# Performance work log

Measured on AMD Instinct MI355X. Metric: run time of the kernel, lower is better.

## Reference

```python
import jax, jax.numpy as jnp
import numpy as np

N = 50000   # nodes
F = 128     # num_features (per branch)
E = 800000  # edges
G = 16      # graphs in batch
T = 3       # blocks per branch


def setup_inputs() -> dict:
    key = jax.random.key(0)
    ks = jax.random.split(key, 32)
    s = 0.05
    d = {}
    d["x"] = jax.random.normal(ks[0], (N, 2 * F), jnp.float32)
    d["edge_index"] = jax.random.randint(ks[1], (2, E), 0, N)
    d["edge_weight"] = jax.random.uniform(ks[2], (E,), jnp.float32)
    d["batch"] = jnp.sort(jax.random.randint(ks[3], (N,), 0, G))
    d["states"] = jax.random.randint(ks[4], (N,), 0, 2).astype(jnp.float32)

    def w(k, shape):
        return jax.random.normal(k, shape, jnp.float32) * s

    for i, p in enumerate(["p1", "p2"]):
        b = 5 + i * 5
        d[f"{p}_a0"] = w(ks[b], (T,))            # alpha0: Linear(1,1,bias=False) weight per block
        d[f"{p}_a1W"] = w(ks[b + 1], (T, F, F))    # alpha1 weight
        d[f"{p}_a1b"] = w(ks[b + 2], (T, F))       # alpha1 bias
        d[f"{p}_linW"] = w(ks[b + 3], (T, F, F))   # conv.lin weight
        d[f"{p}_linb"] = w(ks[b + 4], (T, F))      # conv.lin bias
    d["beta0_W"] = w(ks[15], (F, F))
    d["beta1_W"] = w(ks[16], (F, F))
    d["beta2_W"] = w(ks[17], (F, 2 * F))
    d["beta2_b"] = w(ks[18], (F,))
    d["gamma0_W"] = w(ks[19], (F, F))
    d["gamma1_W"] = w(ks[20], (F, F))
    d["gamma2_W"] = w(ks[21], (F, F))
    d["gamma3_W"] = w(ks[22], (3 * F // 2, 3 * F))
    d["gamma4_W"] = w(ks[23], (1, 3 * F // 2))
    d["gamma4_b"] = w(ks[24], (1,))
    return d


def _lrelu(v):
    return jax.nn.leaky_relu(v, 0.2)


def _block(x, states, a0, a1W, a1b, linW, linb, src, dst, ew):
    # x = lrelu(alpha1(x + alpha0(states)))
    h = _lrelu((x + states[:, None] * a0) @ a1W.T + a1b)
    # CustomGCNConv: lin then edge-weighted gather/scatter-add (source->target)
    h = h @ linW.T + linb
    msg = ew[:, None] * h[src]  # [E, F]
    return jax.ops.segment_sum(msg, dst, num_segments=x.shape[0])


def reference(x, edge_index, edge_weight, batch, states,
              p1_a0, p1_a1W, p1_a1b, p1_linW, p1_linb,
              p2_a0, p2_a1W, p2_a1b, p2_linW, p2_linb,
              beta0_W, beta1_W, beta2_W, beta2_b,
              gamma0_W, gamma1_W, gamma2_W, gamma3_W, gamma4_W, gamma4_b):
    Fh = x.shape[1] // 2
    x1, x2 = x[:, :Fh], x[:, Fh:]
    s0, s1 = edge_index[0], edge_index[1]
    x1s = jnp.zeros_like(x1)
    x2s = jnp.zeros_like(x2)
    for t in range(T):
        # branch1 uses reversed edges edge_index[[1,0]]
        x1 = _lrelu(_block(x1, states, p1_a0[t], p1_a1W[t], p1_a1b[t],
                           p1_linW[t], p1_linb[t], s1, s0, edge_weight))
        x2 = _lrelu(_block(x2, states, p2_a0[t], p2_a1W[t], p2_a1b[t],
                           p2_linW[t], p2_linb[t], s0, s1, edge_weight))
        x1s = x1s + x1
        x2s = x2s + x2
    xc = _lrelu(jnp.concatenate([x1s @ beta0_W.T, x2s @ beta1_W.T], -1) @ beta2_W.T + beta2_b)
    sel = (states == 1.0)[:, None]
    # per-graph pooled sums broadcast back to nodes (== repeat_interleave since batch is sorted)
    x_s = jax.ops.segment_sum(jnp.where(sel, xc, 0.0), batch, num_segments=G)[batch]
    x_sum = jax.ops.segment_sum(xc, batch, num_segments=G)[batch]
    h = jnp.concatenate([xc @ gamma0_W.T, x_s @ gamma1_W.T, x_sum @ gamma2_W.T], -1)
    h = _lrelu(h @ gamma3_W.T)
    return (h @ gamma4_W.T + gamma4_b).reshape(-1)
```

## Files before the change

kernel.cpp:

```cpp
#include <hip/hip_runtime.h>

typedef short s8v __attribute__((ext_vector_type(8)));
typedef float f32x4 __attribute__((ext_vector_type(4)));

#define LRELU(v) ((v) > 0.f ? (v) : 0.2f * (v))

constexpr int NBK = 391;
constexpr int TILE = 8192;
constexpr int CAP = 4096;

__device__ __forceinline__ float b2f(unsigned short b) {
  return __uint_as_float(((unsigned int)b) << 16);
}
__device__ __forceinline__ unsigned short f2b(float f) {
  unsigned int x = __float_as_uint(f);
  x += 0x7fffu + ((x >> 16) & 1u);
  return (unsigned short)(x >> 16);
}
__device__ __forceinline__ unsigned int pack2(float lo, float hi) {
  return ((unsigned int)f2b(hi) << 16) | (unsigned int)f2b(lo);
}

struct BArgs {
  const unsigned short* A1[2];
  const unsigned short* A2[2];
  int ldA1, ldA2, K1;
  const unsigned short* W[2];
  const float* bias[2];
  const float* a0p[2];
  const float* rowsum[2];
  unsigned short* C[2];
  const float* states;
  int N, K;
};

template<int FOUT, int ACT, bool HAS_BIAS, bool HAS_STATES>
__global__ __launch_bounds__(256) void bgemm(BArgs ba)
{
  constexpr int NF = FOUT / 16;
  __shared__ __align__(16) unsigned short Ws[FOUT * 128];
  const int d = blockIdx.y;
  const unsigned short* __restrict__ A1 = ba.A1[d];
  const unsigned short* __restrict__ A2 = ba.A2[d];
  const unsigned short* __restrict__ W  = ba.W[d];
  unsigned short* __restrict__ C = ba.C[d];
  const int N = ba.N, K = ba.K, K1 = ba.K1, ldA1 = ba.ldA1, ldA2 = ba.ldA2;

  const int tid = threadIdx.x;
  const int lane = tid & 63;
  const int w = tid >> 6;
  const int l15 = lane & 15;
  const int g = lane >> 4;
  const int m0 = blockIdx.x * 128;

  f32x4 zero4 = {0.f, 0.f, 0.f, 0.f};
  f32x4 acc[2][NF];
#pragma unroll
  for (int mf = 0; mf < 2; ++mf)
#pragma unroll
    for (int nf = 0; nf < NF; ++nf) acc[mf][nf] = zero4;

  for (int kk = 0; kk < K; kk += 128) {
#pragma unroll
    for (int j = 0; j < NF; ++j) {
      int idx = tid + j * 256;
      int o = idx >> 4, c = idx & 15;
      uint4 v = *(const uint4*)(W + (size_t)o * K + kk + c * 8);
      *(uint4*)&Ws[o * 128 + (c ^ (o & 15)) * 8] = v;
    }
    const unsigned short* Ap; int ldA, koff;
    if (kk < K1) { Ap = A1; ldA = ldA1; koff = kk; }
    else         { Ap = A2; ldA = ldA2; koff = kk - K1; }
    s8v a[2][4];
#pragma unroll
    for (int mf = 0; mf < 2; ++mf) {
      int row = m0 + w * 32 + mf * 16 + l15;
      const unsigned short* ar = Ap + (size_t)row * ldA + koff + g * 8;
#pragma unroll
      for (int ks = 0; ks < 4; ++ks) {
        s8v t = {};
        if (row < N) t = *(const s8v*)(ar + ks * 32);
        a[mf][ks] = t;
      }
    }
    __syncthreads();
#pragma unroll
    for (int ks = 0; ks < 4; ++ks) {
#pragma unroll
      for (int nf = 0; nf < NF; ++nf) {
        int c = ks * 4 + g;
        s8v b = *(const s8v*)&Ws[(nf * 16 + l15) * 128 + (c ^ l15) * 8];
        acc[0][nf] = __builtin_amdgcn_mfma_f32_16x16x32_bf16(a[0][ks], b, acc[0][nf], 0, 0, 0);
        acc[1][nf] = __builtin_amdgcn_mfma_f32_16x16x32_bf16(a[1][ks], b, acc[1][nf], 0, 0, 0);
      }
    }
    if (kk + 128 < K) __syncthreads();
  }

  const float a0 = HAS_STATES ? ba.a0p[d][0] : 0.f;
#pragma unroll
  for (int mf = 0; mf < 2; ++mf) {
#pragma unroll
    for (int r = 0; r < 4; ++r) {
      int row = m0 + w * 32 + mf * 16 + g * 4 + r;
      if (row >= N) continue;
      float sa = HAS_STATES ? ba.states[row] * a0 : 0.f;
      unsigned short* crow = C + (size_t)row * FOUT;
#pragma unroll
      for (int nf = 0; nf < NF; ++nf) {
        int col = nf * 16 + l15;
        float v = acc[mf][nf][r];
        if (HAS_BIAS) v += ba.bias[d][col];
        if (HAS_STATES) v += sa * ba.rowsum[d][col];
        if (ACT) v = LRELU(v);
        crow[col] = f2b(v);
      }
    }
  }
}

struct FArgs {
  const unsigned short* X[2];
  const unsigned short* W1[2];
  const float* b1[2];
  const float* a0p[2];
  const float* rowsum[2];
  const unsigned short* W2[2];
  const float* b2[2];
  unsigned short* H[2];
  const float* states;
  int N;
};

__global__ __launch_bounds__(256) void fused_mlp_kernel(FArgs fa)
{
  __shared__ __align__(16) unsigned short Ws[128 * 128];
  __shared__ __align__(16) unsigned short Tp[128 * 128];
  const int d = blockIdx.y;
  const int tid = threadIdx.x;
  const int lane = tid & 63;
  const int w = tid >> 6;
  const int l15 = lane & 15;
  const int g = lane >> 4;
  const int m0 = blockIdx.x * 128;
  const int N = fa.N;

#pragma unroll
  for (int j = 0; j < 8; ++j) {
    int idx = tid + j * 256;
    int o = idx >> 4, c = idx & 15;
    uint4 v = *(const uint4*)(fa.W1[d] + (size_t)o * 128 + c * 8);
    *(uint4*)&Ws[o * 128 + (c ^ (o & 15)) * 8] = v;
  }
  s8v a[2][4];
#pragma unroll
  for (int mf = 0; mf < 2; ++mf) {
    int row = m0 + w * 32 + mf * 16 + l15;
    const unsigned short* ar = fa.X[d] + (size_t)row * 128 + g * 8;
#pragma unroll
    for (int ks = 0; ks < 4; ++ks) {
      s8v t = {};
      if (row < N) t = *(const s8v*)(ar + ks * 32);
      a[mf][ks] = t;
    }
  }
  f32x4 zero4 = {0.f, 0.f, 0.f, 0.f};
  f32x4 acc[2][8];
#pragma unroll
  for (int mf = 0; mf < 2; ++mf)
#pragma unroll
    for (int nf = 0; nf < 8; ++nf) acc[mf][nf] = zero4;
  __syncthreads();
#pragma unroll
  for (int ks = 0; ks < 4; ++ks) {
#pragma unroll
    for (int nf = 0; nf < 8; ++nf) {
      int c = ks * 4 + g;
      s8v b = *(const s8v*)&Ws[(nf * 16 + l15) * 128 + (c ^ l15) * 8];
      acc[0][nf] = __builtin_amdgcn_mfma_f32_16x16x32_bf16(a[0][ks], b, acc[0][nf], 0, 0, 0);
      acc[1][nf] = __builtin_amdgcn_mfma_f32_16x16x32_bf16(a[1][ks], b, acc[1][nf], 0, 0, 0);
    }
  }
  const float a0 = fa.a0p[d][0];
#pragma unroll
  for (int mf = 0; mf < 2; ++mf) {
#pragma unroll
    for (int r = 0; r < 4; ++r) {
      int lrow = w * 32 + mf * 16 + g * 4 + r;
      int row = m0 + lrow;
      float sa = (row < N) ? fa.states[row] * a0 : 0.f;
#pragma unroll
      for (int nf = 0; nf < 8; ++nf) {
        int col = nf * 16 + l15;
        float v = 0.f;
        if (row < N) {
          v = acc[mf][nf][r] + fa.b1[d][col] + sa * fa.rowsum[d][col];
          v = LRELU(v);
        }
        int cch = col >> 3;
        Tp[lrow * 128 + ((cch ^ (lrow & 15)) << 3) + (col & 7)] = f2b(v);
      }
    }
  }
  __syncthreads();
#pragma unroll
  for (int j = 0; j < 8; ++j) {
    int idx = tid + j * 256;
    int o = idx >> 4, c = idx & 15;
    uint4 v = *(const uint4*)(fa.W2[d] + (size_t)o * 128 + c * 8);
    *(uint4*)&Ws[o * 128 + (c ^ (o & 15)) * 8] = v;
  }
  __syncthreads();
#pragma unroll
  for (int mf = 0; mf < 2; ++mf) {
    int lrow = w * 32 + mf * 16 + l15;
#pragma unroll
    for (int ks = 0; ks < 4; ++ks) {
      int c2 = ks * 4 + g;
      a[mf][ks] = *(const s8v*)&Tp[lrow * 128 + ((c2 ^ (lrow & 15)) << 3)];
    }
  }
#pragma unroll
  for (int mf = 0; mf < 2; ++mf)
#pragma unroll
    for (int nf = 0; nf < 8; ++nf) acc[mf][nf] = zero4;
#pragma unroll
  for (int ks = 0; ks < 4; ++ks) {
#pragma unroll
    for (int nf = 0; nf < 8; ++nf) {
      int c = ks * 4 + g;
      s8v b = *(const s8v*)&Ws[(nf * 16 + l15) * 128 + (c ^ l15) * 8];
      acc[0][nf] = __builtin_amdgcn_mfma_f32_16x16x32_bf16(a[0][ks], b, acc[0][nf], 0, 0, 0);
      acc[1][nf] = __builtin_amdgcn_mfma_f32_16x16x32_bf16(a[1][ks], b, acc[1][nf], 0, 0, 0);
    }
  }
#pragma unroll
  for (int mf = 0; mf < 2; ++mf) {
#pragma unroll
    for (int r = 0; r < 4; ++r) {
      int row = m0 + w * 32 + mf * 16 + g * 4 + r;
      if (row >= N) continue;
      unsigned short* crow = fa.H[d] + (size_t)row * 128;
#pragma unroll
      for (int nf = 0; nf < 8; ++nf) {
        int col = nf * 16 + l15;
        crow[col] = f2b(acc[mf][nf][r] + fa.b2[d][col]);
      }
    }
  }
}

__global__ __launch_bounds__(256) void g3_kernel(
    const unsigned short* __restrict__ wbuf,
    const unsigned short* __restrict__ A16,
    const unsigned short* __restrict__ B16,
    const int* __restrict__ batch,
    const unsigned short* __restrict__ W,
    const float* __restrict__ g4W,
    const float* __restrict__ g4b,
    float* __restrict__ out, int N)
{
  constexpr int NF = 12;
  __shared__ __align__(16) unsigned short Ws[192 * 128];
  const int tid = threadIdx.x;
  const int lane = tid & 63;
  const int w = tid >> 6;
  const int l15 = lane & 15;
  const int g = lane >> 4;
  const int m0 = blockIdx.x * 128;

  f32x4 zero4 = {0.f, 0.f, 0.f, 0.f};
  f32x4 acc[2][NF];
#pragma unroll
  for (int mf = 0; mf < 2; ++mf)
#pragma unroll
    for (int nf = 0; nf < NF; ++nf) acc[mf][nf] = zero4;

  int brow[2];
#pragma unroll
  for (int mf = 0; mf < 2; ++mf) {
    int row = m0 + w * 32 + mf * 16 + l15;
    brow[mf] = (row < N) ? batch[row] : 0;
  }

  for (int kk = 0; kk < 384; kk += 128) {
#pragma unroll
    for (int j = 0; j < NF; ++j) {
      int idx = tid + j * 256;
      int o = idx >> 4, c = idx & 15;
      uint4 v = *(const uint4*)(W + (size_t)o * 384 + kk + c * 8);
      *(uint4*)&Ws[o * 128 + (c ^ (o & 15)) * 8] = v;
    }
    s8v a[2][4];
#pragma unroll
    for (int mf = 0; mf < 2; ++mf) {
      int row = m0 + w * 32 + mf * 16 + l15;
      const unsigned short* ar;
      if (kk == 0)        ar = wbuf + (size_t)row * 128 + g * 8;
      else if (kk == 128) ar = A16 + (size_t)brow[mf] * 128 + g * 8;
      else                ar = B16 + (size_t)brow[mf] * 128 + g * 8;
#pragma unroll
      for (int ks = 0; ks < 4; ++ks) {
        s8v t = {};
        if (row < N) t = *(const s8v*)(ar + ks * 32);
        a[mf][ks] = t;
      }
    }
    __syncthreads();
#pragma unroll
    for (int ks = 0; ks < 4; ++ks) {
#pragma unroll
      for (int nf = 0; nf < NF; ++nf) {
        int c = ks * 4 + g;
        s8v b = *(const s8v*)&Ws[(nf * 16 + l15) * 128 + (c ^ l15) * 8];
        acc[0][nf] = __builtin_amdgcn_mfma_f32_16x16x32_bf16(a[0][ks], b, acc[0][nf], 0, 0, 0);
        acc[1][nf] = __builtin_amdgcn_mfma_f32_16x16x32_bf16(a[1][ks], b, acc[1][nf], 0, 0, 0);
      }
    }
    if (kk < 256) __syncthreads();
  }

  float w4[NF];
#pragma unroll
  for (int nf = 0; nf < NF; ++nf) w4[nf] = g4W[nf * 16 + l15];
  const float gb = g4b[0];

#pragma unroll
  for (int mf = 0; mf < 2; ++mf) {
#pragma unroll
    for (int r = 0; r < 4; ++r) {
      int row = m0 + w * 32 + mf * 16 + g * 4 + r;
      float dot = 0.f;
#pragma unroll
      for (int nf = 0; nf < NF; ++nf) {
        float v = acc[mf][nf][r];
        v = LRELU(v);
        dot += v * w4[nf];
      }
#pragma unroll
      for (int m = 1; m < 16; m <<= 1) dot += __shfl_xor(dot, m, 16);
      if (l15 == 0 && row < N) out[row] = dot + gb;
    }
  }
}

struct CJobs { const float* s[9]; unsigned short* d[9]; int n[9]; };
__global__ void convert_kernel(CJobs jb) {
  int j = blockIdx.y;
  int idx = (blockIdx.x * 256 + threadIdx.x) * 8;
  if (idx >= jb.n[j]) return;
  const float* s = jb.s[j] + idx;
  float4 p0 = *(const float4*)s;
  float4 p1 = *(const float4*)(s + 4);
  uint4 u;
  u.x = pack2(p0.x, p0.y); u.y = pack2(p0.z, p0.w);
  u.z = pack2(p1.x, p1.y); u.w = pack2(p1.z, p1.w);
  *(uint4*)(jb.d[j] + idx) = u;
}

__global__ void rowsum_kernel(const float* __restrict__ a1,
                              const float* __restrict__ a2, float* __restrict__ rs) {
  int j = blockIdx.x;
  const float* src = (j < 3) ? (a1 + (size_t)j * 16384) : (a2 + (size_t)(j - 3) * 16384);
  int o = threadIdx.x;
  float s = 0.f;
  for (int k = 0; k < 128; ++k) s += src[o * 128 + k];
  rs[j * 128 + o] = s;
}

__global__ void init_kernel(const float* __restrict__ x,
                            unsigned short* __restrict__ x1, unsigned short* __restrict__ x2,
                            int n)
{
  int idx = blockIdx.x * blockDim.x + threadIdx.x;
  int total = n * 16;
  for (; idx < total; idx += gridDim.x * blockDim.x) {
    int r = idx >> 4, c = idx & 15;
    const float* xr = x + (size_t)r * 256 + c * 8;
    float4 p0 = *(const float4*)xr;
    float4 p1 = *(const float4*)(xr + 4);
    uint4 u1;
    u1.x = pack2(p0.x, p0.y); u1.y = pack2(p0.z, p0.w);
    u1.z = pack2(p1.x, p1.y); u1.w = pack2(p1.z, p1.w);
    float4 q0 = *(const float4*)(xr + 128);
    float4 q1 = *(const float4*)(xr + 132);
    uint4 u2;
    u2.x = pack2(q0.x, q0.y); u2.y = pack2(q0.z, q0.w);
    u2.z = pack2(q1.x, q1.y); u2.w = pack2(q1.z, q1.w);
    ((uint4*)(x1 + (size_t)r * 128))[c] = u1;
    ((uint4*)(x2 + (size_t)r * 128))[c] = u2;
  }
}

struct S3Args { const unsigned int* a[2]; const unsigned int* b[2]; const unsigned int* c[2];
                unsigned int* o[2]; int n; };
__global__ void sum3_kernel(S3Args s)
{
  int d = blockIdx.y;
  const unsigned int* __restrict__ pa = s.a[d];
  const unsigned int* __restrict__ pb = s.b[d];
  const unsigned int* __restrict__ pc = s.c[d];
  unsigned int* __restrict__ po = s.o[d];
  for (int i = blockIdx.x * 256 + threadIdx.x; i < s.n; i += gridDim.x * 256) {
    unsigned int ua = pa[i], ub = pb[i], uc = pc[i];
    float lo = b2f((unsigned short)ua) + b2f((unsigned short)ub) + b2f((unsigned short)uc);
    float hi = b2f((unsigned short)(ua >> 16)) + b2f((unsigned short)(ub >> 16))
             + b2f((unsigned short)(uc >> 16));
    po[i] = pack2(lo, hi);
  }
}

struct BinArgs {
  const int* s0; const int* s1; const float* ew;
  int* bcur0; int* bcur1;
  unsigned long long* bin0; unsigned long long* bin1;
  int E;
};
__global__ __launch_bounds__(256) void bin_kernel(BinArgs ba)
{
  __shared__ int hist0[NBK], hist1[NBK];
  __shared__ int base0[NBK], base1[NBK];
  const int t = threadIdx.x;
  const int e0 = blockIdx.x * TILE;
  const int e1 = min(e0 + TILE, ba.E);
  for (int i = t; i < NBK; i += 256) { hist0[i] = 0; hist1[i] = 0; }
  __syncthreads();
  for (int e = e0 + t; e < e1; e += 256) {
    atomicAdd(&hist0[ba.s0[e] >> 7], 1);
    atomicAdd(&hist1[ba.s1[e] >> 7], 1);
  }
  __syncthreads();
  for (int i = t; i < NBK; i += 256) {
    int c0 = hist0[i];
    base0[i] = c0 ? atomicAdd(&ba.bcur0[i], c0) : 0;
    int c1 = hist1[i];
    base1[i] = c1 ? atomicAdd(&ba.bcur1[i], c1) : 0;
  }
  __syncthreads();
  for (int i = t; i < NBK; i += 256) { hist0[i] = 0; hist1[i] = 0; }
  __syncthreads();
  for (int e = e0 + t; e < e1; e += 256) {
    int d0 = ba.s0[e], d1 = ba.s1[e];
    unsigned long long wb = (unsigned long long)__float_as_uint(ba.ew[e]) << 32;
    int b0 = d0 >> 7, b1 = d1 >> 7;
    int r0 = base0[b0] + atomicAdd(&hist0[b0], 1);
    if (r0 < CAP)
      ba.bin0[(size_t)b0 * CAP + r0] = wb | (unsigned int)((d0 & 127) << 16) | (unsigned int)d1;
    int r1 = base1[b1] + atomicAdd(&hist1[b1], 1);
    if (r1 < CAP)
      ba.bin1[(size_t)b1 * CAP + r1] = wb | (unsigned int)((d1 & 127) << 16) | (unsigned int)d0;
  }
}

struct BScanArgs { const int* cnt[2]; int* bbase[2]; };
__global__ __launch_bounds__(128) void bscan_kernel(BScanArgs a)
{
  __shared__ int ld[2][NBK];
  int wid = threadIdx.x >> 6, lane = threadIdx.x & 63;
  for (int i = lane; i < NBK; i += 64) ld[wid][i] = a.cnt[wid][i];
  __syncthreads();
  if (lane == 0) {
    int acc = 0;
    for (int i = 0; i < NBK; ++i) { int v = ld[wid][i]; ld[wid][i] = acc; acc += v; }
    a.bbase[wid][NBK] = acc;
  }
  __syncthreads();
  for (int i = lane; i < NBK; i += 64) a.bbase[wid][i] = ld[wid][i];
}

struct RArgs {
  const int* bbase[2];
  const unsigned long long* bin[2];
  unsigned int* comb[2];
  int* row[2];
  int n;
};
__global__ __launch_bounds__(256) void reorder_kernel(RArgs ra)
{
  const int d = blockIdx.y;
  const int b = blockIdx.x;
  const unsigned long long* __restrict__ bin = ra.bin[d] + (size_t)b * CAP;
  unsigned int* __restrict__ comb = ra.comb[d];
  int* __restrict__ row = ra.row[d];
  const int nb = b * 128;
  const int ne = min(nb + 128, ra.n);
  const int t = threadIdx.x;
  __shared__ int lcnt[128];
  __shared__ int lcur[128];
  __shared__ int wtot[4];
  if (t < 128) lcnt[t] = 0;
  const int span_beg = ra.bbase[d][b];
  const int span_end = ra.bbase[d][b + 1];
  const int cnt = span_end - span_beg;
  __syncthreads();
  for (int i = t; i < cnt; i += 256) {
    int nl = ((unsigned int)bin[i] >> 16) & 127;
    atomicAdd(&lcnt[nl], 1);
  }
  __syncthreads();
  int lane = t & 63, wv = t >> 6;
  int v = (t < 128) ? lcnt[t] : 0;
  int sc = v;
#pragma unroll
  for (int off = 1; off < 64; off <<= 1) {
    int u = __shfl_up(sc, off, 64);
    if (lane >= off) sc += u;
  }
  if (lane == 63) wtot[wv] = sc;
  __syncthreads();
  int excl = sc - v + ((wv == 1) ? wtot[0] : 0);
  if (t < 128) {
    lcur[t] = excl;
    if (nb + t < ne) row[nb + t] = span_beg + excl;
  }
  if (b == NBK - 1 && t == 0) row[ra.n] = span_end;
  __syncthreads();
  for (int i = t; i < cnt; i += 256) {
    unsigned long long r = bin[i];
    unsigned int lo = (unsigned int)r;
    float w = __uint_as_float((unsigned int)(r >> 32));
    int nl = (lo >> 16) & 127;
    int slot = atomicAdd(&lcur[nl], 1);
    comb[span_beg + slot] = (lo & 0xffffu) | ((unsigned int)f2b(w) << 16);
  }
}

struct GArgs {
  const int* rowstart[2];
  const unsigned int* comb[2];
  const unsigned short* h[2];
  unsigned short* xout[2];
  int n;
};
__global__ void gather_kernel(GArgs ga)
{
  int gw = blockIdx.x * (blockDim.x >> 6) + (threadIdx.x >> 6);
  int lane = threadIdx.x & 63;
  if (gw >= 2 * ga.n) return;
  int dir = (gw >= ga.n) ? 1 : 0;
  int node = gw - dir * ga.n;
  const int* __restrict__ rowstart = ga.rowstart[dir];
  const unsigned int* __restrict__ comb = ga.comb[dir];
  const unsigned int* __restrict__ h = (const unsigned int*)ga.h[dir];
  int beg = rowstart[node], end = rowstart[node + 1];
  float a0 = 0.f, a1 = 0.f;
  for (int p = beg; p < end; p += 16) {
    unsigned int cc[16];
    unsigned int uu[16];
#pragma unroll
    for (int i = 0; i < 16; ++i) {
      int pi = p + i;
      cc[i] = (pi < end) ? comb[pi] : 0u;
    }
#pragma unroll
    for (int i = 0; i < 16; ++i)
      uu[i] = h[(size_t)(cc[i] & 0xffffu) * 64 + lane];
#pragma unroll
    for (int i = 0; i < 16; ++i) {
      float wv = b2f((unsigned short)(cc[i] >> 16));
      a0 += wv * b2f((unsigned short)uu[i]);
      a1 += wv * b2f((unsigned short)(uu[i] >> 16));
    }
  }
  float v0 = LRELU(a0), v1 = LRELU(a1);
  unsigned int* xo = (unsigned int*)(ga.xout[dir] + (size_t)node * 128);
  xo[lane] = pack2(v0, v1);
}

__global__ __launch_bounds__(256) void segsum_kernel(
    const unsigned short* __restrict__ xc, const int* __restrict__ batch,
    const float* __restrict__ states,
    float* __restrict__ gsel, float* __restrict__ gsum, int n)
{
  int slot = threadIdx.x >> 6;
  int lane = threadIdx.x & 63;
  int r0 = blockIdx.x * 128 + slot * 32;
  if (r0 >= n) return;
  int r1 = min(r0 + 32, n);
  const unsigned int* __restrict__ xcu = (const unsigned int*)xc;
  float sel0 = 0.f, sel1 = 0.f, sum0 = 0.f, sum1 = 0.f;
  int cur = batch[r0];
  for (int r = r0; r < r1; r += 4) {
    unsigned int u[4]; int bb[4]; float st[4];
#pragma unroll
    for (int i = 0; i < 4; ++i) {
      int ri = min(r + i, r1 - 1);
      u[i] = xcu[(size_t)ri * 64 + lane];
      bb[i] = batch[ri];
      st[i] = states[ri];
    }
    int m = min(4, r1 - r);
#pragma unroll
    for (int i = 0; i < 4; ++i) {
      if (i >= m) break;
      if (bb[i] != cur) {
        atomicAdd(&gsel[cur * 128 + lane * 2], sel0);
        atomicAdd(&gsel[cur * 128 + lane * 2 + 1], sel1);
        atomicAdd(&gsum[cur * 128 + lane * 2], sum0);
        atomicAdd(&gsum[cur * 128 + lane * 2 + 1], sum1);
        sel0 = sel1 = sum0 = sum1 = 0.f;
        cur = bb[i];
      }
      float lo = b2f((unsigned short)u[i]);
      float hi = b2f((unsigned short)(u[i] >> 16));
      sum0 += lo; sum1 += hi;
      if (st[i] == 1.0f) { sel0 += lo; sel1 += hi; }
    }
  }
  atomicAdd(&gsel[cur * 128 + lane * 2], sel0);
  atomicAdd(&gsel[cur * 128 + lane * 2 + 1], sel1);
  atomicAdd(&gsum[cur * 128 + lane * 2], sum0);
  atomicAdd(&gsum[cur * 128 + lane * 2 + 1], sum1);
}

__global__ void small16_kernel(const float* __restrict__ gsel, const float* __restrict__ gsum,
                               const float* __restrict__ g1W, const float* __restrict__ g2W,
                               unsigned short* __restrict__ A16, unsigned short* __restrict__ B16)
{
  int r = blockIdx.x, t = threadIdx.x, o = t & 127;
  const float* src = (t < 128) ? gsel : gsum;
  const float* Wm  = (t < 128) ? g1W : g2W;
  float acc = 0.f;
  for (int k = 0; k < 128; ++k) acc += src[r * 128 + k] * Wm[o * 128 + k];
  unsigned short* dst = (t < 128) ? A16 : B16;
  dst[r * 128 + o] = f2b(acc);
}

extern "C" void kernel_launch(void* const* d_in, const int* in_sizes, int n_in,
                              void* d_out, int out_size, void* d_ws, size_t ws_size,
                              hipStream_t stream)
{
  const int N = 50000, F = 128, E = 800000, G = 16, T = 3;
  const float* x      = (const float*)d_in[0];
  const int*   ei     = (const int*)d_in[1];
  const int*   s0     = ei;
  const int*   s1     = ei + E;
  const float* ew     = (const float*)d_in[2];
  const int*   batch  = (const int*)d_in[3];
  const float* states = (const float*)d_in[4];
  const float* p_a0[2]   = {(const float*)d_in[5],  (const float*)d_in[10]};
  const float* p_a1W[2]  = {(const float*)d_in[6],  (const float*)d_in[11]};
  const float* p_a1b[2]  = {(const float*)d_in[7],  (const float*)d_in[12]};
  const float* p_linW[2] = {(const float*)d_in[8],  (const float*)d_in[13]};
  const float* p_linb[2] = {(const float*)d_in[9],  (const float*)d_in[14]};
  const float* beta0W = (const float*)d_in[15];
  const float* beta1W = (const float*)d_in[16];
  const float* beta2W = (const float*)d_in[17];
  const float* beta2b = (const float*)d_in[18];
  const float* g0W = (const float*)d_in[19];
  const float* g1W = (const float*)d_in[20];
  const float* g2W = (const float*)d_in[21];
  const float* g3W = (const float*)d_in[22];
  const float* g4W = (const float*)d_in[23];
  const float* g4b = (const float*)d_in[24];
  float* out = (float*)d_out;

  char* p = (char*)d_ws;
  auto alloc = [&](size_t bytes) {
    char* r = p;
    p += (bytes + 255) & ~(size_t)255;
    return r;
  };
  const size_t NFb2 = (size_t)N * F * sizeof(unsigned short);
  unsigned short* X1[3] = {(unsigned short*)alloc(NFb2), (unsigned short*)alloc(NFb2),
                           (unsigned short*)alloc(NFb2)};
  unsigned short* X2[3] = {(unsigned short*)alloc(NFb2), (unsigned short*)alloc(NFb2),
                           (unsigned short*)alloc(NFb2)};
  unsigned short* TMP0 = (unsigned short*)alloc(NFb2);
  unsigned short* TMP1 = (unsigned short*)alloc(NFb2);
  unsigned short* HH0  = (unsigned short*)alloc(NFb2);
  unsigned short* HH1  = (unsigned short*)alloc(NFb2);
  int*   row0 = (int*)alloc((size_t)(N + 1) * 4);
  int*   row1 = (int*)alloc((size_t)(N + 1) * 4);
  int*   bbase0 = (int*)alloc((size_t)(NBK + 1) * 4);
  int*   bbase1 = (int*)alloc((size_t)(NBK + 1) * 4);
  int*   bcur0 = (int*)alloc((size_t)NBK * 4);
  int*   bcur1 = (int*)alloc((size_t)NBK * 4);
  unsigned long long* bin0 = (unsigned long long*)alloc((size_t)NBK * CAP * 8);
  unsigned long long* bin1 = (unsigned long long*)alloc((size_t)NBK * CAP * 8);
  unsigned int* comb0 = (unsigned int*)alloc((size_t)E * 4);
  unsigned int* comb1 = (unsigned int*)alloc((size_t)E * 4);
  float* gsel = (float*)alloc((size_t)G * F * 4);
  float* gsum = (float*)alloc((size_t)G * F * 4);
  unsigned short* A16b = (unsigned short*)alloc((size_t)G * F * 2);
  unsigned short* B16b = (unsigned short*)alloc((size_t)G * F * 2);
  unsigned short* wreg = (unsigned short*)alloc((size_t)352256 * 2);
  float* rs = (float*)alloc((size_t)6 * 128 * 4);

  unsigned short* a1Wb[2]  = {wreg + 0,      wreg + 49152};
  unsigned short* linWb[2] = {wreg + 98304,  wreg + 147456};
  unsigned short* b0b = wreg + 196608;
  unsigned short* b1b = wreg + 212992;
  unsigned short* b2b = wreg + 229376;
  unsigned short* g0b = wreg + 262144;
  unsigned short* g3b = wreg + 278528;

  const dim3 blk256(256);
  const int GX = (N + 127) / 128;
  const int KBIG = 1 << 30;
  const int EB = (E + TILE - 1) / TILE;

  hipMemsetAsync(bcur0, 0, (size_t)NBK * 4, stream);
  hipMemsetAsync(bcur1, 0, (size_t)NBK * 4, stream);
  BinArgs bna;
  bna.s0 = s0; bna.s1 = s1; bna.ew = ew;
  bna.bcur0 = bcur0; bna.bcur1 = bcur1;
  bna.bin0 = bin0; bna.bin1 = bin1;
  bna.E = E;
  bin_kernel<<<EB, blk256, 0, stream>>>(bna);
  BScanArgs bsa;
  bsa.cnt[0] = bcur0; bsa.cnt[1] = bcur1;
  bsa.bbase[0] = bbase0; bsa.bbase[1] = bbase1;
  bscan_kernel<<<1, 128, 0, stream>>>(bsa);
  RArgs ra;
  ra.bbase[0] = bbase0; ra.bbase[1] = bbase1;
  ra.bin[0] = bin0; ra.bin[1] = bin1;
  ra.comb[0] = comb0; ra.comb[1] = comb1;
  ra.row[0] = row0; ra.row[1] = row1;
  ra.n = N;
  reorder_kernel<<<dim3(NBK, 2), blk256, 0, stream>>>(ra);

  CJobs jb;
  jb.s[0] = p_a1W[0];  jb.d[0] = a1Wb[0];  jb.n[0] = 49152;
  jb.s[1] = p_a1W[1];  jb.d[1] = a1Wb[1];  jb.n[1] = 49152;
  jb.s[2] = p_linW[0]; jb.d[2] = linWb[0]; jb.n[2] = 49152;
  jb.s[3] = p_linW[1]; jb.d[3] = linWb[1]; jb.n[3] = 49152;
  jb.s[4] = beta0W;    jb.d[4] = b0b;      jb.n[4] = 16384;
  jb.s[5] = beta1W;    jb.d[5] = b1b;      jb.n[5] = 16384;
  jb.s[6] = beta2W;    jb.d[6] = b2b;      jb.n[6] = 32768;
  jb.s[7] = g0W;       jb.d[7] = g0b;      jb.n[7] = 16384;
  jb.s[8] = g3W;       jb.d[8] = g3b;      jb.n[8] = 73728;
  convert_kernel<<<dim3(36, 9), blk256, 0, stream>>>(jb);
  rowsum_kernel<<<6, 128, 0, stream>>>(p_a1W[0], p_a1W[1], rs);
  init_kernel<<<3125, blk256, 0, stream>>>(x, X1[0], X2[0], N);

  for (int t = 0; t < T; ++t) {
    int rv = t % 3, wv = (t + 1) % 3;

    FArgs fa;
    fa.X[0] = X1[rv];  fa.X[1] = X2[rv];
    fa.W1[0] = a1Wb[0] + t * 16384;  fa.W1[1] = a1Wb[1] + t * 16384;
    fa.b1[0] = p_a1b[0] + t * F;     fa.b1[1] = p_a1b[1] + t * F;
    fa.a0p[0] = p_a0[0] + t;         fa.a0p[1] = p_a0[1] + t;
    fa.rowsum[0] = rs + t * 128;     fa.rowsum[1] = rs + (3 + t) * 128;
    fa.W2[0] = linWb[0] + t * 16384; fa.W2[1] = linWb[1] + t * 16384;
    fa.b2[0] = p_linb[0] + t * F;    fa.b2[1] = p_linb[1] + t * F;
    fa.H[0] = HH0;  fa.H[1] = HH1;
    fa.states = states;  fa.N = N;
    fused_mlp_kernel<<<dim3(GX, 2), blk256, 0, stream>>>(fa);

    GArgs ga;
    ga.rowstart[0] = row0; ga.rowstart[1] = row1;
    ga.comb[0] = comb0;    ga.comb[1] = comb1;
    ga.h[0] = HH0;         ga.h[1] = HH1;
    ga.xout[0] = X1[wv];   ga.xout[1] = X2[wv];
    ga.n = N;
    gather_kernel<<<(2 * N + 3) / 4, blk256, 0, stream>>>(ga);
  }

  S3Args s3;
  s3.a[0] = (const unsigned int*)X1[0]; s3.b[0] = (const unsigned int*)X1[1];
  s3.c[0] = (const unsigned int*)X1[2]; s3.o[0] = (unsigned int*)TMP0;
  s3.a[1] = (const unsigned int*)X2[0]; s3.b[1] = (const unsigned int*)X2[1];
  s3.c[1] = (const unsigned int*)X2[2]; s3.o[1] = (unsigned int*)TMP1;
  s3.n = N * 64;
  sum3_kernel<<<dim3(2048, 2), blk256, 0, stream>>>(s3);

  BArgs bu;
  bu.A1[0] = TMP0; bu.A2[0] = TMP0; bu.A1[1] = TMP1; bu.A2[1] = TMP1;
  bu.ldA1 = 128; bu.ldA2 = 128; bu.K1 = KBIG;
  bu.W[0] = b0b; bu.W[1] = b1b;
  bu.bias[0] = nullptr; bu.bias[1] = nullptr;
  bu.a0p[0] = nullptr; bu.a0p[1] = nullptr;
  bu.rowsum[0] = nullptr; bu.rowsum[1] = nullptr;
  bu.C[0] = HH0; bu.C[1] = HH1;
  bu.states = nullptr; bu.N = N; bu.K = 128;
  bgemm<128, 0, false, false><<<dim3(GX, 2), blk256, 0, stream>>>(bu);

  BArgs b2a;
  b2a.A1[0] = HH0; b2a.A2[0] = HH1; b2a.A1[1] = nullptr; b2a.A2[1] = nullptr;
  b2a.ldA1 = 128; b2a.ldA2 = 128; b2a.K1 = 128;
  b2a.W[0] = b2b; b2a.W[1] = nullptr;
  b2a.bias[0] = beta2b; b2a.bias[1] = nullptr;
  b2a.a0p[0] = nullptr; b2a.a0p[1] = nullptr;
  b2a.rowsum[0] = nullptr; b2a.rowsum[1] = nullptr;
  b2a.C[0] = TMP0; b2a.C[1] = nullptr;
  b2a.states = nullptr; b2a.N = N; b2a.K = 256;
  bgemm<128, 1, true, false><<<dim3(GX, 1), blk256, 0, stream>>>(b2a);

  hipMemsetAsync(gsel, 0, (size_t)G * F * 4, stream);
  hipMemsetAsync(gsum, 0, (size_t)G * F * 4, stream);
  segsum_kernel<<<GX, blk256, 0, stream>>>(TMP0, batch, states, gsel, gsum, N);
  small16_kernel<<<G, blk256, 0, stream>>>(gsel, gsum, g1W, g2W, A16b, B16b);

  BArgs g0a;
  g0a.A1[0] = TMP0; g0a.A2[0] = TMP0; g0a.A1[1] = nullptr; g0a.A2[1] = nullptr;
  g0a.ldA1 = 128; g0a.ldA2 = 128; g0a.K1 = KBIG;
  g0a.W[0] = g0b; g0a.W[1] = nullptr;
  g0a.bias[0] = nullptr; g0a.bias[1] = nullptr;
  g0a.a0p[0] = nullptr; g0a.a0p[1] = nullptr;
  g0a.rowsum[0] = nullptr; g0a.rowsum[1] = nullptr;
  g0a.C[0] = TMP1; g0a.C[1] = nullptr;
  g0a.states = nullptr; g0a.N = N; g0a.K = 128;
  bgemm<128, 0, false, false><<<dim3(GX, 1), blk256, 0, stream>>>(g0a);

  g3_kernel<<<GX, blk256, 0, stream>>>(TMP1, A16b, B16b, batch, g3b, g4W, g4b, out, N);
}
```

Measured before the change: 468.2 us.

## Fuse tail GEMMs and fold block-sum into last gather

Three tail changes. The three-way branch sum moves into the final gather kernel, which adds the two earlier block outputs before writing. The two per-branch beta GEMMs and the beta2 GEMM become one kernel that keeps intermediates in shared memory. The gamma0 GEMM is fused into g3_kernel through an LDS tile. This removes several kernel launches and multiple N×128 bf16 round trips to global memory, at the cost of larger shared-memory use per block (about 96 KB in the beta kernel) and possibly lower occupancy.

```diff
diff --git a/kernel.cpp b/kernel.cpp
--- a/kernel.cpp
+++ b/kernel.cpp
@@ -19,104 +19,6 @@
 }
 __device__ __forceinline__ unsigned int pack2(float lo, float hi) {
   return ((unsigned int)f2b(hi) << 16) | (unsigned int)f2b(lo);
-}
-
-struct BArgs {
-  const unsigned short* A1[2];
-  const unsigned short* A2[2];
-  int ldA1, ldA2, K1;
-  const unsigned short* W[2];
-  const float* bias[2];
-  const float* a0p[2];
-  const float* rowsum[2];
-  unsigned short* C[2];
-  const float* states;
-  int N, K;
-};
-
-template<int FOUT, int ACT, bool HAS_BIAS, bool HAS_STATES>
-__global__ __launch_bounds__(256) void bgemm(BArgs ba)
-{
-  constexpr int NF = FOUT / 16;
-  __shared__ __align__(16) unsigned short Ws[FOUT * 128];
-  const int d = blockIdx.y;
-  const unsigned short* __restrict__ A1 = ba.A1[d];
-  const unsigned short* __restrict__ A2 = ba.A2[d];
-  const unsigned short* __restrict__ W  = ba.W[d];
-  unsigned short* __restrict__ C = ba.C[d];
-  const int N = ba.N, K = ba.K, K1 = ba.K1, ldA1 = ba.ldA1, ldA2 = ba.ldA2;
-
-  const int tid = threadIdx.x;
-  const int lane = tid & 63;
-  const int w = tid >> 6;
-  const int l15 = lane & 15;
-  const int g = lane >> 4;
-  const int m0 = blockIdx.x * 128;
-
-  f32x4 zero4 = {0.f, 0.f, 0.f, 0.f};
-  f32x4 acc[2][NF];
-#pragma unroll
-  for (int mf = 0; mf < 2; ++mf)
-#pragma unroll
-    for (int nf = 0; nf < NF; ++nf) acc[mf][nf] = zero4;
-
-  for (int kk = 0; kk < K; kk += 128) {
-#pragma unroll
-    for (int j = 0; j < NF; ++j) {
-      int idx = tid + j * 256;
-      int o = idx >> 4, c = idx & 15;
-      uint4 v = *(const uint4*)(W + (size_t)o * K + kk + c * 8);
-      *(uint4*)&Ws[o * 128 + (c ^ (o & 15)) * 8] = v;
-    }
-    const unsigned short* Ap; int ldA, koff;
-    if (kk < K1) { Ap = A1; ldA = ldA1; koff = kk; }
-    else         { Ap = A2; ldA = ldA2; koff = kk - K1; }
-    s8v a[2][4];
-#pragma unroll
-    for (int mf = 0; mf < 2; ++mf) {
-      int row = m0 + w * 32 + mf * 16 + l15;
-      const unsigned short* ar = Ap + (size_t)row * ldA + koff + g * 8;
-#pragma unroll
-      for (int ks = 0; ks < 4; ++ks) {
-        s8v t = {};
-        if (row < N) t = *(const s8v*)(ar + ks * 32);
-        a[mf][ks] = t;
-      }
-    }
-    __syncthreads();
-#pragma unroll
-    for (int ks = 0; ks < 4; ++ks) {
-#pragma unroll
-      for (int nf = 0; nf < NF; ++nf) {
-        int c = ks * 4 + g;
-        s8v b = *(const s8v*)&Ws[(nf * 16 + l15) * 128 + (c ^ l15) * 8];
-        acc[0][nf] = __builtin_amdgcn_mfma_f32_16x16x32_bf16(a[0][ks], b, acc[0][nf], 0, 0, 0);
-        acc[1][nf] = __builtin_amdgcn_mfma_f32_16x16x32_bf16(a[1][ks], b, acc[1][nf], 0, 0, 0);
-      }
-    }
-    if (kk + 128 < K) __syncthreads();
-  }
-
-  const float a0 = HAS_STATES ? ba.a0p[d][0] : 0.f;
-#pragma unroll
-  for (int mf = 0; mf < 2; ++mf) {
-#pragma unroll
-    for (int r = 0; r < 4; ++r) {
-      int row = m0 + w * 32 + mf * 16 + g * 4 + r;
-      if (row >= N) continue;
-      float sa = HAS_STATES ? ba.states[row] * a0 : 0.f;
-      unsigned short* crow = C + (size_t)row * FOUT;
-#pragma unroll
-      for (int nf = 0; nf < NF; ++nf) {
-        int col = nf * 16 + l15;
-        float v = acc[mf][nf][r];
-        if (HAS_BIAS) v += ba.bias[d][col];
-        if (HAS_STATES) v += sa * ba.rowsum[d][col];
-        if (ACT) v = LRELU(v);
-        crow[col] = f2b(v);
-      }
-    }
-  }
 }
 
 struct FArgs {
@@ -250,60 +152,257 @@
   }
 }
 
-__global__ __launch_bounds__(256) void g3_kernel(
-    const unsigned short* __restrict__ wbuf,
-    const unsigned short* __restrict__ A16,
-    const unsigned short* __restrict__ B16,
-    const int* __restrict__ batch,
-    const unsigned short* __restrict__ W,
-    const float* __restrict__ g4W,
-    const float* __restrict__ g4b,
-    float* __restrict__ out, int N)
-{
-  constexpr int NF = 12;
-  __shared__ __align__(16) unsigned short Ws[192 * 128];
+struct PBArgs {
+  const unsigned short* U1; const unsigned short* U2;
+  const unsigned short* Wb0; const unsigned short* Wb1;
+  const unsigned short* Wb2;
+  const float* bias;
+  unsigned short* XC;
+  int N;
+};
+
+__global__ __launch_bounds__(256) void fused_beta_kernel(PBArgs pa)
+{
+  __shared__ __align__(16) unsigned short Ws[128 * 128];
+  __shared__ __align__(16) unsigned short Tp[128 * 256];
   const int tid = threadIdx.x;
   const int lane = tid & 63;
   const int w = tid >> 6;
   const int l15 = lane & 15;
   const int g = lane >> 4;
   const int m0 = blockIdx.x * 128;
-
+  const int N = pa.N;
   f32x4 zero4 = {0.f, 0.f, 0.f, 0.f};
-  f32x4 acc[2][NF];
-#pragma unroll
-  for (int mf = 0; mf < 2; ++mf)
-#pragma unroll
-    for (int nf = 0; nf < NF; ++nf) acc[mf][nf] = zero4;
-
-  int brow[2];
-#pragma unroll
-  for (int mf = 0; mf < 2; ++mf) {
-    int row = m0 + w * 32 + mf * 16 + l15;
-    brow[mf] = (row < N) ? batch[row] : 0;
-  }
-
-  for (int kk = 0; kk < 384; kk += 128) {
-#pragma unroll
-    for (int j = 0; j < NF; ++j) {
+  s8v a[2][4];
+  f32x4 acc[2][8];
+
+#pragma unroll
+  for (int ph = 0; ph < 2; ++ph) {
+    const unsigned short* Wsrc = ph ? pa.Wb1 : pa.Wb0;
+    const unsigned short* Usrc = ph ? pa.U2 : pa.U1;
+#pragma unroll
+    for (int j = 0; j < 8; ++j) {
       int idx = tid + j * 256;
       int o = idx >> 4, c = idx & 15;
-      uint4 v = *(const uint4*)(W + (size_t)o * 384 + kk + c * 8);
+      uint4 v = *(const uint4*)(Wsrc + (size_t)o * 128 + c * 8);
       *(uint4*)&Ws[o * 128 + (c ^ (o & 15)) * 8] = v;
     }
-    s8v a[2][4];
 #pragma unroll
     for (int mf = 0; mf < 2; ++mf) {
       int row = m0 + w * 32 + mf * 16 + l15;
-      const unsigned short* ar;
-      if (kk == 0)        ar = wbuf + (size_t)row * 128 + g * 8;
-      else if (kk == 128) ar = A16 + (size_t)brow[mf] * 128 + g * 8;
-      else                ar = B16 + (size_t)brow[mf] * 128 + g * 8;
+      const unsigned short* ar = Usrc + (size_t)row * 128 + g * 8;
 #pragma unroll
       for (int ks = 0; ks < 4; ++ks) {
         s8v t = {};
         if (row < N) t = *(const s8v*)(ar + ks * 32);
         a[mf][ks] = t;
+      }
+    }
+#pragma unroll
+    for (int mf = 0; mf < 2; ++mf)
+#pragma unroll
+      for (int nf = 0; nf < 8; ++nf) acc[mf][nf] = zero4;
+    __syncthreads();
+#pragma unroll
+    for (int ks = 0; ks < 4; ++ks) {
+#pragma unroll
+      for (int nf = 0; nf < 8; ++nf) {
+        int c = ks * 4 + g;
+        s8v b = *(const s8v*)&Ws[(nf * 16 + l15) * 128 + (c ^ l15) * 8];
+        acc[0][nf] = __builtin_amdgcn_mfma_f32_16x16x32_bf16(a[0][ks], b, acc[0][nf], 0, 0, 0);
+        acc[1][nf] = __builtin_amdgcn_mfma_f32_16x16x32_bf16(a[1][ks], b, acc[1][nf], 0, 0, 0);
+      }
+    }
+#pragma unroll
+    for (int mf = 0; mf < 2; ++mf) {
+#pragma unroll
+      for (int r = 0; r < 4; ++r) {
+        int lrow = w * 32 + mf * 16 + g * 4 + r;
+        int row = m0 + lrow;
+#pragma unroll
+        for (int nf = 0; nf < 8; ++nf) {
+          int col = nf * 16 + l15;
+          float v = (row < N) ? acc[mf][nf][r] : 0.f;
+          int cch = (ph << 4) + (col >> 3);
+          Tp[lrow * 256 + ((cch ^ (lrow & 15)) << 3) + (col & 7)] = f2b(v);
+        }
+      }
+    }
+    __syncthreads();
+  }
+
+  f32x4 accf[2][8];
+#pragma unroll
+  for (int mf = 0; mf < 2; ++mf)
+#pragma unroll
+    for (int nf = 0; nf < 8; ++nf) accf[mf][nf] = zero4;
+#pragma unroll
+  for (int half = 0; half < 2; ++half) {
+#pragma unroll
+    for (int j = 0; j < 8; ++j) {
+      int idx = tid + j * 256;
+      int o = idx >> 4, c = idx & 15;
+      uint4 v = *(const uint4*)(pa.Wb2 + (size_t)o * 256 + half * 128 + c * 8);
+      *(uint4*)&Ws[o * 128 + (c ^ (o & 15)) * 8] = v;
+    }
+#pragma unroll
+    for (int mf = 0; mf < 2; ++mf) {
+      int lrow = w * 32 + mf * 16 + l15;
+#pragma unroll
+      for (int ks = 0; ks < 4; ++ks) {
+        int cch = (half << 4) + ks * 4 + g;
+        a[mf][ks] = *(const s8v*)&Tp[lrow * 256 + ((cch ^ (lrow & 15)) << 3)];
+      }
+    }
+    __syncthreads();
+#pragma unroll
+    for (int ks = 0; ks < 4; ++ks) {
+#pragma unroll
+      for (int nf = 0; nf < 8; ++nf) {
+        int c = ks * 4 + g;
+        s8v b = *(const s8v*)&Ws[(nf * 16 + l15) * 128 + (c ^ l15) * 8];
+        accf[0][nf] = __builtin_amdgcn_mfma_f32_16x16x32_bf16(a[0][ks], b, accf[0][nf], 0, 0, 0);
+        accf[1][nf] = __builtin_amdgcn_mfma_f32_16x16x32_bf16(a[1][ks], b, accf[1][nf], 0, 0, 0);
+      }
+    }
+    __syncthreads();
+  }
+#pragma unroll
+  for (int mf = 0; mf < 2; ++mf) {
+#pragma unroll
+    for (int r = 0; r < 4; ++r) {
+      int row = m0 + w * 32 + mf * 16 + g * 4 + r;
+      if (row >= N) continue;
+      unsigned short* crow = pa.XC + (size_t)row * 128;
+#pragma unroll
+      for (int nf = 0; nf < 8; ++nf) {
+        int col = nf * 16 + l15;
+        float v = accf[mf][nf][r] + pa.bias[col];
+        crow[col] = f2b(LRELU(v));
+      }
+    }
+  }
+}
+
+__global__ __launch_bounds__(256) void g3_kernel(
+    const unsigned short* __restrict__ xc,
+    const unsigned short* __restrict__ A16,
+    const unsigned short* __restrict__ B16,
+    const int* __restrict__ batch,
+    const unsigned short* __restrict__ W0,
+    const unsigned short* __restrict__ W3,
+    const float* __restrict__ g4W,
+    const float* __restrict__ g4b,
+    float* __restrict__ out, int N)
+{
+  constexpr int NF = 12;
+  __shared__ __align__(16) unsigned short Ws[192 * 128];
+  __shared__ __align__(16) unsigned short Tp[128 * 128];
+  const int tid = threadIdx.x;
+  const int lane = tid & 63;
+  const int w = tid >> 6;
+  const int l15 = lane & 15;
+  const int g = lane >> 4;
+  const int m0 = blockIdx.x * 128;
+
+  f32x4 zero4 = {0.f, 0.f, 0.f, 0.f};
+  s8v a[2][4];
+
+#pragma unroll
+  for (int j = 0; j < 8; ++j) {
+    int idx = tid + j * 256;
+    int o = idx >> 4, c = idx & 15;
+    uint4 v = *(const uint4*)(W0 + (size_t)o * 128 + c * 8);
+    *(uint4*)&Ws[o * 128 + (c ^ (o & 15)) * 8] = v;
+  }
+#pragma unroll
+  for (int mf = 0; mf < 2; ++mf) {
+    int row = m0 + w * 32 + mf * 16 + l15;
+    const unsigned short* ar = xc + (size_t)row * 128 + g * 8;
+#pragma unroll
+    for (int ks = 0; ks < 4; ++ks) {
+      s8v t = {};
+      if (row < N) t = *(const s8v*)(ar + ks * 32);
+      a[mf][ks] = t;
+    }
+  }
+  {
+    f32x4 acc1[2][8];
+#pragma unroll
+    for (int mf = 0; mf < 2; ++mf)
+#pragma unroll
+      for (int nf = 0; nf < 8; ++nf) acc1[mf][nf] = zero4;
+    __syncthreads();
+#pragma unroll
+    for (int ks = 0; ks < 4; ++ks) {
+#pragma unroll
+      for (int nf = 0; nf < 8; ++nf) {
+        int c = ks * 4 + g;
+        s8v b = *(const s8v*)&Ws[(nf * 16 + l15) * 128 + (c ^ l15) * 8];
+        acc1[0][nf] = __builtin_amdgcn_mfma_f32_16x16x32_bf16(a[0][ks], b, acc1[0][nf], 0, 0, 0);
+        acc1[1][nf] = __builtin_amdgcn_mfma_f32_16x16x32_bf16(a[1][ks], b, acc1[1][nf], 0, 0, 0);
+      }
+    }
+#pragma unroll
+    for (int mf = 0; mf < 2; ++mf) {
+#pragma unroll
+      for (int r = 0; r < 4; ++r) {
+        int lrow = w * 32 + mf * 16 + g * 4 + r;
+        int row = m0 + lrow;
+#pragma unroll
+        for (int nf = 0; nf < 8; ++nf) {
+          int col = nf * 16 + l15;
+          float v = (row < N) ? acc1[mf][nf][r] : 0.f;
+          int cch = col >> 3;
+          Tp[lrow * 128 + ((cch ^ (lrow & 15)) << 3) + (col & 7)] = f2b(v);
+        }
+      }
+    }
+  }
+  __syncthreads();
+
+  f32x4 acc[2][NF];
+#pragma unroll
+  for (int mf = 0; mf < 2; ++mf)
+#pragma unroll
+    for (int nf = 0; nf < NF; ++nf) acc[mf][nf] = zero4;
+
+  int brow[2];
+#pragma unroll
+  for (int mf = 0; mf < 2; ++mf) {
+    int row = m0 + w * 32 + mf * 16 + l15;
+    brow[mf] = (row < N) ? batch[row] : 0;
+  }
+
+  for (int kk = 0; kk < 384; kk += 128) {
+#pragma unroll
+    for (int j = 0; j < NF; ++j) {
+      int idx = tid + j * 256;
+      int o = idx >> 4, c = idx & 15;
+      uint4 v = *(const uint4*)(W3 + (size_t)o * 384 + kk + c * 8);
+      *(uint4*)&Ws[o * 128 + (c ^ (o & 15)) * 8] = v;
+    }
+    if (kk == 0) {
+#pragma unroll
+      for (int mf = 0; mf < 2; ++mf) {
+        int lrow = w * 32 + mf * 16 + l15;
+#pragma unroll
+        for (int ks = 0; ks < 4; ++ks) {
+          int c2 = ks * 4 + g;
+          a[mf][ks] = *(const s8v*)&Tp[lrow * 128 + ((c2 ^ (lrow & 15)) << 3)];
+        }
+      }
+    } else {
+#pragma unroll
+      for (int mf = 0; mf < 2; ++mf) {
+        int row = m0 + w * 32 + mf * 16 + l15;
+        const unsigned short* ar = ((kk == 128) ? A16 : B16) + (size_t)brow[mf] * 128 + g * 8;
+#pragma unroll
+        for (int ks = 0; ks < 4; ++ks) {
+          s8v t = {};
+          if (row < N) t = *(const s8v*)(ar + ks * 32);
+          a[mf][ks] = t;
+        }
       }
     }
     __syncthreads();
@@ -392,24 +491,6 @@
   }
 }
 
-struct S3Args { const unsigned int* a[2]; const unsigned int* b[2]; const unsigned int* c[2];
-                unsigned int* o[2]; int n; };
-__global__ void sum3_kernel(S3Args s)
-{
-  int d = blockIdx.y;
-  const unsigned int* __restrict__ pa = s.a[d];
-  const unsigned int* __restrict__ pb = s.b[d];
-  const unsigned int* __restrict__ pc = s.c[d];
-  unsigned int* __restrict__ po = s.o[d];
-  for (int i = blockIdx.x * 256 + threadIdx.x; i < s.n; i += gridDim.x * 256) {
-    unsigned int ua = pa[i], ub = pb[i], uc = pc[i];
-    float lo = b2f((unsigned short)ua) + b2f((unsigned short)ub) + b2f((unsigned short)uc);
-    float hi = b2f((unsigned short)(ua >> 16)) + b2f((unsigned short)(ub >> 16))
-             + b2f((unsigned short)(uc >> 16));
-    po[i] = pack2(lo, hi);
-  }
-}
-
 struct BinArgs {
   const int* s0; const int* s1; const float* ew;
   int* bcur0; int* bcur1;
@@ -530,6 +611,8 @@
   const unsigned int* comb[2];
   const unsigned short* h[2];
   unsigned short* xout[2];
+  const unsigned int* add1[2];
+  const unsigned int* add2[2];
   int n;
 };
 __global__ void gather_kernel(GArgs ga)
@@ -564,6 +647,12 @@
   }
   float v0 = LRELU(a0), v1 = LRELU(a1);
   unsigned int* xo = (unsigned int*)(ga.xout[dir] + (size_t)node * 128);
+  if (ga.add1[0]) {
+    unsigned int ua = ga.add1[dir][(size_t)node * 64 + lane];
+    unsigned int ub = ga.add2[dir][(size_t)node * 64 + lane];
+    v0 += b2f((unsigned short)ua) + b2f((unsigned short)ub);
+    v1 += b2f((unsigned short)(ua >> 16)) + b2f((unsigned short)(ub >> 16));
+  }
   xo[lane] = pack2(v0, v1);
 }
 
@@ -697,7 +786,6 @@
 
   const dim3 blk256(256);
   const int GX = (N + 127) / 128;
-  const int KBIG = 1 << 30;
   const int EB = (E + TILE - 1) / TILE;
 
   hipMemsetAsync(bcur0, 0, (size_t)NBK * 4, stream);
@@ -753,56 +841,29 @@
     ga.rowstart[0] = row0; ga.rowstart[1] = row1;
     ga.comb[0] = comb0;    ga.comb[1] = comb1;
     ga.h[0] = HH0;         ga.h[1] = HH1;
-    ga.xout[0] = X1[wv];   ga.xout[1] = X2[wv];
+    if (t == T - 1) {
+      ga.xout[0] = TMP0;  ga.xout[1] = TMP1;
+      ga.add1[0] = (const unsigned int*)X1[1];  ga.add1[1] = (const unsigned int*)X2[1];
+      ga.add2[0] = (const unsigned int*)X1[2];  ga.add2[1] = (const unsigned int*)X2[2];
+    } else {
+      ga.xout[0] = X1[wv];  ga.xout[1] = X2[wv];
+      ga.add1[0] = nullptr; ga.add1[1] = nullptr;
+      ga.add2[0] = nullptr; ga.add2[1] = nullptr;
+    }
     ga.n = N;
     gather_kernel<<<(2 * N + 3) / 4, blk256, 0, stream>>>(ga);
   }
 
-  S3Args s3;
-  s3.a[0] = (const unsigned int*)X1[0]; s3.b[0] = (const unsigned int*)X1[1];
-  s3.c[0] = (const unsigned int*)X1[2]; s3.o[0] = (unsigned int*)TMP0;
-  s3.a[1] = (const unsigned int*)X2[0]; s3.b[1] = (const unsigned int*)X2[1];
-  s3.c[1] = (const unsigned int*)X2[2]; s3.o[1] = (unsigned int*)TMP1;
-  s3.n = N * 64;
-  sum3_kernel<<<dim3(2048, 2), blk256, 0, stream>>>(s3);
-
-  BArgs bu;
-  bu.A1[0] = TMP0; bu.A2[0] = TMP0; bu.A1[1] = TMP1; bu.A2[1] = TMP1;
-  bu.ldA1 = 128; bu.ldA2 = 128; bu.K1 = KBIG;
-  bu.W[0] = b0b; bu.W[1] = b1b;
-  bu.bias[0] = nullptr; bu.bias[1] = nullptr;
-  bu.a0p[0] = nullptr; bu.a0p[1] = nullptr;
-  bu.rowsum[0] = nullptr; bu.rowsum[1] = nullptr;
-  bu.C[0] = HH0; bu.C[1] = HH1;
-  bu.states = nullptr; bu.N = N; bu.K = 128;
-  bgemm<128, 0, false, false><<<dim3(GX, 2), blk256, 0, stream>>>(bu);
-
-  BArgs b2a;
-  b2a.A1[0] = HH0; b2a.A2[0] = HH1; b2a.A1[1] = nullptr; b2a.A2[1] = nullptr;
-  b2a.ldA1 = 128; b2a.ldA2 = 128; b2a.K1 = 128;
-  b2a.W[0] = b2b; b2a.W[1] = nullptr;
-  b2a.bias[0] = beta2b; b2a.bias[1] = nullptr;
-  b2a.a0p[0] = nullptr; b2a.a0p[1] = nullptr;
-  b2a.rowsum[0] = nullptr; b2a.rowsum[1] = nullptr;
-  b2a.C[0] = TMP0; b2a.C[1] = nullptr;
-  b2a.states = nullptr; b2a.N = N; b2a.K = 256;
-  bgemm<128, 1, true, false><<<dim3(GX, 1), blk256, 0, stream>>>(b2a);
+  PBArgs pb;
+  pb.U1 = TMP0; pb.U2 = TMP1;
+  pb.Wb0 = b0b; pb.Wb1 = b1b; pb.Wb2 = b2b;
+  pb.bias = beta2b; pb.XC = HH0; pb.N = N;
+  fused_beta_kernel<<<GX, blk256, 0, stream>>>(pb);
 
   hipMemsetAsync(gsel, 0, (size_t)G * F * 4, stream);
   hipMemsetAsync(gsum, 0, (size_t)G * F * 4, stream);
-  segsum_kernel<<<GX, blk256, 0, stream>>>(TMP0, batch, states, gsel, gsum, N);
+  segsum_kernel<<<GX, blk256, 0, stream>>>(HH0, batch, states, gsel, gsum, N);
   small16_kernel<<<G, blk256, 0, stream>>>(gsel, gsum, g1W, g2W, A16b, B16b);
 
-  BArgs g0a;
-  g0a.A1[0] = TMP0; g0a.A2[0] = TMP0; g0a.A1[1] = nullptr; g0a.A2[1] = nullptr;
-  g0a.ldA1 = 128; g0a.ldA2 = 128; g0a.K1 = KBIG;
-  g0a.W[0] = g0b; g0a.W[1] = nullptr;
-  g0a.bias[0] = nullptr; g0a.bias[1] = nullptr;
-  g0a.a0p[0] = nullptr; g0a.a0p[1] = nullptr;
-  g0a.rowsum[0] = nullptr; g0a.rowsum[1] = nullptr;
-  g0a.C[0] = TMP1; g0a.C[1] = nullptr;
-  g0a.states = nullptr; g0a.N = N; g0a.K = 128;
-  bgemm<128, 0, false, false><<<dim3(GX, 1), blk256, 0, stream>>>(g0a);
-
-  g3_kernel<<<GX, blk256, 0, stream>>>(TMP1, A16b, B16b, batch, g3b, g4W, g4b, out, N);
-}
+  g3_kernel<<<GX, blk256, 0, stream>>>(HH0, A16b, B16b, batch, g0b, g3b, g4W, g4b, out, N);
+}
```

After: 456.0 us. -2.6%, faster.
